# Kernel tuning notes

Measured on AMD Instinct MI355X. Metric: run time of the kernel, lower is better.

Reference implementation:

```python
import jax, jax.numpy as jnp
import numpy as np

N_NODES = 50000
IN_SIZE = 64
LAYER_SIZE = 64
N_EDGES = 800000


def setup_inputs() -> dict:
    key = jax.random.key(0)
    k1, k2, k3, k4 = jax.random.split(key, 4)
    x = jax.random.normal(k1, (N_NODES, IN_SIZE), dtype=jnp.float32)
    edge_index = jax.random.randint(k2, (2, N_EDGES), 0, N_NODES, dtype=jnp.int64)
    # nn.Linear(in_size*2, layer_size): weight [out, in], bias [out]
    lim = 1.0 / np.sqrt(2 * IN_SIZE)
    W = jax.random.uniform(k3, (LAYER_SIZE, 2 * IN_SIZE), minval=-lim, maxval=lim, dtype=jnp.float32)
    b = jax.random.uniform(k4, (LAYER_SIZE,), minval=-lim, maxval=lim, dtype=jnp.float32)
    return {"x": x, "edge_index": edge_index, "W": W, "b": b}


def reference(x, edge_index, W, b):
    # PyG convention: edge_index[0] = source j, edge_index[1] = target i
    src = edge_index[0]
    dst = edge_index[1]
    x_j = x[src]                      # [E, F]
    x_i = x[dst]                      # [E, F]
    msg_in = jnp.concatenate([x_i, x_j - x_i], axis=-1)  # [E, 2F]
    msg = msg_in @ W.T + b            # [E, layer_size]
    # mean aggregation over target nodes (0 for isolated nodes, like PyG)
    summed = jax.ops.segment_sum(msg, dst, num_segments=N_NODES)  # [N, layer_size]
    ones = jnp.ones((msg.shape[0],), dtype=msg.dtype)
    count = jax.ops.segment_sum(ones, dst, num_segments=N_NODES)
    out = summed / jnp.maximum(count, 1.0)[:, None]
    return out
```

## Files before the change

kernel.cpp:

```cpp
#include <hip/hip_runtime.h>
#include <hip/hip_bf16.h>

#define NN 50000
#define FF 64
#define EE 800000
#define CAP 64
#define NCHUNK 3125

__global__ __launch_bounds__(256, 4) void prep_kernel(
    const float* __restrict__ x, const float* __restrict__ W,
    const float* __restrict__ b, __hip_bfloat16* __restrict__ xbh,
    float* __restrict__ p, int* __restrict__ cursor)
{
    for (int i = blockIdx.x * 256 + threadIdx.x; i < NN; i += gridDim.x * 256)
        cursor[i] = 0;

    __shared__ float WA[64][65];
    __shared__ float W2s[64][65];
    __shared__ float bl[64];
    for (int i = threadIdx.x; i < 4096; i += 256) {
        int r = i >> 6, c = i & 63;
        float w2 = W[r * 128 + 64 + c];
        WA[r][c]  = W[r * 128 + c] - w2;
        W2s[r][c] = w2;
    }
    if (threadIdx.x < 64) bl[threadIdx.x] = b[threadIdx.x];
    __syncthreads();

    const int wid = threadIdx.x >> 6, lane = threadIdx.x & 63;
    const int nw = gridDim.x * 4;
    for (int n = blockIdx.x * 4 + wid; n < NN; n += nw) {
        const float4* xr = (const float4*)(x + (size_t)n * FF);
        float a1 = bl[lane], a2 = 0.f;
        #pragma unroll 4
        for (int kk = 0; kk < 16; ++kk) {
            float4 xk = xr[kk];
            a1 += WA[lane][4*kk+0] * xk.x + WA[lane][4*kk+1] * xk.y
                + WA[lane][4*kk+2] * xk.z + WA[lane][4*kk+3] * xk.w;
            a2 += W2s[lane][4*kk+0] * xk.x + W2s[lane][4*kk+1] * xk.y
                + W2s[lane][4*kk+2] * xk.z + W2s[lane][4*kk+3] * xk.w;
        }
        p  [(size_t)n * FF + lane] = a1;
        xbh[(size_t)n * FF + lane] = __float2bfloat16(a2);
    }
}

__global__ __launch_bounds__(256) void fill_kernel(const int* __restrict__ idx,
                                                   int* __restrict__ cursor,
                                                   int* __restrict__ ssrc) {
    int p     = blockIdx.x & 7;
    int chunk = blockIdx.x >> 3;
    int e = chunk * 256 + threadIdx.x;
    if (e >= EE) return;
    int dst = idx[EE + e];
    if ((dst & 7) != p) return;
    int src = idx[e];
    int pos = atomicAdd(&cursor[dst], 1);
    if (pos < CAP) ssrc[(dst << 6) + pos] = src;
}

__global__ __launch_bounds__(256) void aggregate_kernel(
    const ushort* __restrict__ xbh, const int* __restrict__ cursor,
    const int* __restrict__ ssrc, float* __restrict__ out)
{
    int tid = blockIdx.x * 256 + threadIdx.x;
    int n = tid >> 3;
    if (n >= NN) return;
    int q = tid & 7;
    int c = cursor[n];
    int cg = (c < CAP) ? c : CAP;
    const int* row = ssrc + ((size_t)n << 6);

    float s[8] = {0,0,0,0,0,0,0,0};
    #define ACC(u)  do { \
        s[0] += __uint_as_float((u).x << 16); s[1] += __uint_as_float((u).x & 0xffff0000u); \
        s[2] += __uint_as_float((u).y << 16); s[3] += __uint_as_float((u).y & 0xffff0000u); \
        s[4] += __uint_as_float((u).z << 16); s[5] += __uint_as_float((u).z & 0xffff0000u); \
        s[6] += __uint_as_float((u).w << 16); s[7] += __uint_as_float((u).w & 0xffff0000u); } while (0)

    int j = 0;
    for (; j + 4 <= cg; j += 4) {
        int e0 = row[j], e1 = row[j+1], e2 = row[j+2], e3 = row[j+3];
        uint4 u0 = *(const uint4*)(xbh + (size_t)e0 * FF + q * 8);
        uint4 u1 = *(const uint4*)(xbh + (size_t)e1 * FF + q * 8);
        uint4 u2 = *(const uint4*)(xbh + (size_t)e2 * FF + q * 8);
        uint4 u3 = *(const uint4*)(xbh + (size_t)e3 * FF + q * 8);
        ACC(u0); ACC(u1); ACC(u2); ACC(u3);
    }
    for (; j < cg; ++j) {
        uint4 u = *(const uint4*)(xbh + (size_t)row[j] * FF + q * 8);
        ACC(u);
    }
    #undef ACC

    float* op = out + (size_t)n * FF + q * 8;
    if (c > 0) {
        float inv = 1.0f / (float)c;
        float4 p0 = *(const float4*)op;
        float4 p1 = *(const float4*)(op + 4);
        float4 r0, r1;
        r0.x = p0.x + s[0]*inv; r0.y = p0.y + s[1]*inv;
        r0.z = p0.z + s[2]*inv; r0.w = p0.w + s[3]*inv;
        r1.x = p1.x + s[4]*inv; r1.y = p1.y + s[5]*inv;
        r1.z = p1.z + s[6]*inv; r1.w = p1.w + s[7]*inv;
        *(float4*)op = r0;
        *(float4*)(op + 4) = r1;
    } else {
        float4 z = {0,0,0,0};
        *(float4*)op = z;
        *(float4*)(op + 4) = z;
    }
}

extern "C" void kernel_launch(void* const* d_in, const int* in_sizes, int n_in,
                              void* d_out, int out_size, void* d_ws, size_t ws_size,
                              hipStream_t stream) {
    const float* x   = (const float*)d_in[0];
    const int*   idx = (const int*)d_in[1];
    const float* W   = (const float*)d_in[2];
    const float* b   = (const float*)d_in[3];
    float* out = (float*)d_out;

    int*            cursor = (int*)d_ws;
    int*            ssrc   = cursor + NN;
    __hip_bfloat16* xbh    = (__hip_bfloat16*)(ssrc + (size_t)NN * CAP);

    prep_kernel     <<<1024, 256, 0, stream>>>(x, W, b, xbh, out, cursor);
    fill_kernel     <<<NCHUNK * 8, 256, 0, stream>>>(idx, cursor, ssrc);
    aggregate_kernel<<<(NN * 8 + 255) / 256, 256, 0, stream>>>((const ushort*)xbh, cursor, ssrc, out);
}
```

Measured before the change: 162.2 us.

## Aggregate raw bf16 features first, then apply linear layer with MFMA GEMM

Reorders the computation to mean-aggregate the bf16-converted node features before the linear transform. The 128x64 projection is then done once per node by a separate MFMA bf16 GEMM kernel over the concatenated [x, mean(x_j)] rows. The prep kernel becomes a plain bf16 conversion instead of a per-node FP32 dot-product loop, and the aggregate kernel no longer reads and writes the FP32 output. This adds a kernel launch and an intermediate bf16 buffer, and it rounds x, W and the aggregated means to bf16, which lowers precision.

```diff
diff --git a/kernel.cpp b/kernel.cpp
--- a/kernel.cpp
+++ b/kernel.cpp
@@ -1,47 +1,43 @@
 #include <hip/hip_runtime.h>
-#include <hip/hip_bf16.h>
 
 #define NN 50000
 #define FF 64
 #define EE 800000
 #define CAP 64
 #define NCHUNK 3125
+#define NSTRIP 3125
 
-__global__ __launch_bounds__(256, 4) void prep_kernel(
+typedef short bf16x8 __attribute__((ext_vector_type(8)));
+typedef float f32x4  __attribute__((ext_vector_type(4)));
+
+static __device__ __forceinline__ unsigned bf16rne(float f) {
+    unsigned u = __float_as_uint(f);
+    return (u + 0x7FFFu + ((u >> 16) & 1u)) >> 16;
+}
+static __device__ __forceinline__ unsigned packbf(float lo, float hi) {
+    return bf16rne(lo) | (bf16rne(hi) << 16);
+}
+
+__global__ __launch_bounds__(256) void prep_kernel(
     const float* __restrict__ x, const float* __restrict__ W,
-    const float* __restrict__ b, __hip_bfloat16* __restrict__ xbh,
-    float* __restrict__ p, int* __restrict__ cursor)
+    ushort* __restrict__ xh, ushort* __restrict__ wcat, int* __restrict__ cursor)
 {
-    for (int i = blockIdx.x * 256 + threadIdx.x; i < NN; i += gridDim.x * 256)
-        cursor[i] = 0;
-
-    __shared__ float WA[64][65];
-    __shared__ float W2s[64][65];
-    __shared__ float bl[64];
-    for (int i = threadIdx.x; i < 4096; i += 256) {
-        int r = i >> 6, c = i & 63;
-        float w2 = W[r * 128 + 64 + c];
-        WA[r][c]  = W[r * 128 + c] - w2;
-        W2s[r][c] = w2;
+    int tid = blockIdx.x * 256 + threadIdx.x;
+    int gs  = gridDim.x * 256;
+    for (int i = tid; i < NN; i += gs) cursor[i] = 0;
+    for (int i = tid; i < 64 * 64; i += gs) {
+        int f = i >> 6, k = (i & 63) * 2;
+        float lo = (k < 64) ? (W[f * 128 + k]     - W[f * 128 + 64 + k])     : W[f * 128 + k];
+        float hi = (k < 63) ? (W[f * 128 + k + 1] - W[f * 128 + 64 + k + 1]) : W[f * 128 + k + 1];
+        ((unsigned*)wcat)[i] = packbf(lo, hi);
     }
-    if (threadIdx.x < 64) bl[threadIdx.x] = b[threadIdx.x];
-    __syncthreads();
-
-    const int wid = threadIdx.x >> 6, lane = threadIdx.x & 63;
-    const int nw = gridDim.x * 4;
-    for (int n = blockIdx.x * 4 + wid; n < NN; n += nw) {
-        const float4* xr = (const float4*)(x + (size_t)n * FF);
-        float a1 = bl[lane], a2 = 0.f;
-        #pragma unroll 4
-        for (int kk = 0; kk < 16; ++kk) {
-            float4 xk = xr[kk];
-            a1 += WA[lane][4*kk+0] * xk.x + WA[lane][4*kk+1] * xk.y
-                + WA[lane][4*kk+2] * xk.z + WA[lane][4*kk+3] * xk.w;
-            a2 += W2s[lane][4*kk+0] * xk.x + W2s[lane][4*kk+1] * xk.y
-                + W2s[lane][4*kk+2] * xk.z + W2s[lane][4*kk+3] * xk.w;
-        }
-        p  [(size_t)n * FF + lane] = a1;
-        xbh[(size_t)n * FF + lane] = __float2bfloat16(a2);
+    for (int i = tid; i < NN * FF / 8; i += gs) {
+        const float4* xr = (const float4*)x + (size_t)i * 2;
+        float4 v0 = xr[0], v1 = xr[1];
+        uint4 o;
+        o.x = packbf(v0.x, v0.y); o.y = packbf(v0.z, v0.w);
+        o.z = packbf(v1.x, v1.y); o.w = packbf(v1.z, v1.w);
+        ((uint4*)xh)[i] = o;
     }
 }
 
@@ -59,9 +55,9 @@
     if (pos < CAP) ssrc[(dst << 6) + pos] = src;
 }
 
-__global__ __launch_bounds__(256) void aggregate_kernel(
-    const ushort* __restrict__ xbh, const int* __restrict__ cursor,
-    const int* __restrict__ ssrc, float* __restrict__ out)
+__global__ __launch_bounds__(256) void gather_kernel(
+    const ushort* __restrict__ xh, const int* __restrict__ cursor,
+    const int* __restrict__ ssrc, ushort* __restrict__ sh)
 {
     int tid = blockIdx.x * 256 + threadIdx.x;
     int n = tid >> 3;
@@ -77,38 +73,76 @@
         s[2] += __uint_as_float((u).y << 16); s[3] += __uint_as_float((u).y & 0xffff0000u); \
         s[4] += __uint_as_float((u).z << 16); s[5] += __uint_as_float((u).z & 0xffff0000u); \
         s[6] += __uint_as_float((u).w << 16); s[7] += __uint_as_float((u).w & 0xffff0000u); } while (0)
-
     int j = 0;
     for (; j + 4 <= cg; j += 4) {
         int e0 = row[j], e1 = row[j+1], e2 = row[j+2], e3 = row[j+3];
-        uint4 u0 = *(const uint4*)(xbh + (size_t)e0 * FF + q * 8);
-        uint4 u1 = *(const uint4*)(xbh + (size_t)e1 * FF + q * 8);
-        uint4 u2 = *(const uint4*)(xbh + (size_t)e2 * FF + q * 8);
-        uint4 u3 = *(const uint4*)(xbh + (size_t)e3 * FF + q * 8);
+        uint4 u0 = *(const uint4*)(xh + (size_t)e0 * FF + q * 8);
+        uint4 u1 = *(const uint4*)(xh + (size_t)e1 * FF + q * 8);
+        uint4 u2 = *(const uint4*)(xh + (size_t)e2 * FF + q * 8);
+        uint4 u3 = *(const uint4*)(xh + (size_t)e3 * FF + q * 8);
         ACC(u0); ACC(u1); ACC(u2); ACC(u3);
     }
     for (; j < cg; ++j) {
-        uint4 u = *(const uint4*)(xbh + (size_t)row[j] * FF + q * 8);
+        uint4 u = *(const uint4*)(xh + (size_t)row[j] * FF + q * 8);
         ACC(u);
     }
     #undef ACC
 
-    float* op = out + (size_t)n * FF + q * 8;
-    if (c > 0) {
-        float inv = 1.0f / (float)c;
-        float4 p0 = *(const float4*)op;
-        float4 p1 = *(const float4*)(op + 4);
-        float4 r0, r1;
-        r0.x = p0.x + s[0]*inv; r0.y = p0.y + s[1]*inv;
-        r0.z = p0.z + s[2]*inv; r0.w = p0.w + s[3]*inv;
-        r1.x = p1.x + s[4]*inv; r1.y = p1.y + s[5]*inv;
-        r1.z = p1.z + s[6]*inv; r1.w = p1.w + s[7]*inv;
-        *(float4*)op = r0;
-        *(float4*)(op + 4) = r1;
-    } else {
-        float4 z = {0,0,0,0};
-        *(float4*)op = z;
-        *(float4*)(op + 4) = z;
+    float inv = (c > 0) ? 1.0f / (float)c : 0.0f;
+    uint4 o;
+    o.x = packbf(s[0]*inv, s[1]*inv); o.y = packbf(s[2]*inv, s[3]*inv);
+    o.z = packbf(s[4]*inv, s[5]*inv); o.w = packbf(s[6]*inv, s[7]*inv);
+    *(uint4*)(sh + (size_t)n * FF + q * 8) = o;
+}
+
+__global__ __launch_bounds__(256) void gemm_kernel(
+    const ushort* __restrict__ xh, const ushort* __restrict__ sh,
+    const ushort* __restrict__ wcat, const float* __restrict__ bias,
+    const int* __restrict__ cursor, float* __restrict__ out)
+{
+    const int wid = threadIdx.x >> 6, lane = threadIdx.x & 63;
+    const int r16 = lane & 15, g = lane >> 4;
+
+    bf16x8 bf[4][4];
+    #pragma unroll
+    for (int nt = 0; nt < 4; ++nt)
+        #pragma unroll
+        for (int ks = 0; ks < 4; ++ks)
+            bf[nt][ks] = *(const bf16x8*)(wcat + (nt * 16 + r16) * 128 + ks * 32 + g * 8);
+    float bv[4];
+    #pragma unroll
+    for (int nt = 0; nt < 4; ++nt) bv[nt] = bias[nt * 16 + r16];
+
+    for (int strip = blockIdx.x * 4 + wid; strip < NSTRIP; strip += gridDim.x * 4) {
+        int n0 = strip * 16;
+        const ushort* ax = xh + (size_t)(n0 + r16) * FF + g * 8;
+        const ushort* as = sh + (size_t)(n0 + r16) * FF + g * 8;
+        bf16x8 a0 = *(const bf16x8*)(ax);
+        bf16x8 a1 = *(const bf16x8*)(ax + 32);
+        bf16x8 a2 = *(const bf16x8*)(as);
+        bf16x8 a3 = *(const bf16x8*)(as + 32);
+
+        f32x4 acc[4] = {{0,0,0,0},{0,0,0,0},{0,0,0,0},{0,0,0,0}};
+        #pragma unroll
+        for (int nt = 0; nt < 4; ++nt) {
+            acc[nt] = __builtin_amdgcn_mfma_f32_16x16x32_bf16(a0, bf[nt][0], acc[nt], 0, 0, 0);
+            acc[nt] = __builtin_amdgcn_mfma_f32_16x16x32_bf16(a1, bf[nt][1], acc[nt], 0, 0, 0);
+            acc[nt] = __builtin_amdgcn_mfma_f32_16x16x32_bf16(a2, bf[nt][2], acc[nt], 0, 0, 0);
+            acc[nt] = __builtin_amdgcn_mfma_f32_16x16x32_bf16(a3, bf[nt][3], acc[nt], 0, 0, 0);
+        }
+
+        int4 c4 = *(const int4*)(cursor + n0 + g * 4);
+        int cc[4] = {c4.x, c4.y, c4.z, c4.w};
+        #pragma unroll
+        for (int r = 0; r < 4; ++r) {
+            int n = n0 + g * 4 + r;
+            float* op = out + (size_t)n * FF + r16;
+            bool nz = cc[r] > 0;
+            op[0]  = nz ? acc[0][r] + bv[0] : 0.f;
+            op[16] = nz ? acc[1][r] + bv[1] : 0.f;
+            op[32] = nz ? acc[2][r] + bv[2] : 0.f;
+            op[48] = nz ? acc[3][r] + bv[3] : 0.f;
+        }
     }
 }
 
@@ -121,11 +155,14 @@
     const float* b   = (const float*)d_in[3];
     float* out = (float*)d_out;
 
-    int*            cursor = (int*)d_ws;
-    int*            ssrc   = cursor + NN;
-    __hip_bfloat16* xbh    = (__hip_bfloat16*)(ssrc + (size_t)NN * CAP);
+    int*    cursor = (int*)d_ws;
+    int*    ssrc   = cursor + NN;
+    ushort* xh     = (ushort*)(ssrc + (size_t)NN * CAP);
+    ushort* sh     = xh + (size_t)NN * FF;
+    ushort* wcat   = sh + (size_t)NN * FF;
 
-    prep_kernel     <<<1024, 256, 0, stream>>>(x, W, b, xbh, out, cursor);
-    fill_kernel     <<<NCHUNK * 8, 256, 0, stream>>>(idx, cursor, ssrc);
-    aggregate_kernel<<<(NN * 8 + 255) / 256, 256, 0, stream>>>((const ushort*)xbh, cursor, ssrc, out);
+    prep_kernel  <<<1563, 256, 0, stream>>>(x, W, xh, wcat, cursor);
+    fill_kernel  <<<NCHUNK * 8, 256, 0, stream>>>(idx, cursor, ssrc);
+    gather_kernel<<<(NN * 8 + 255) / 256, 256, 0, stream>>>(xh, cursor, ssrc, sh);
+    gemm_kernel  <<<391, 256, 0, stream>>>(xh, sh, wcat, b, cursor, out);
 }
```

New measurement: 142.6 us. -12.1%, faster.
